# Kernel optimization log

Measured on AMD Instinct MI355X. Metric: run time of the kernel, lower is better.

The kernel has to match this reference:

```python
import jax, jax.numpy as jnp
import numpy as np
import math

HIDDEN = 2048
N_HEADS = 16
N_KV_HEADS = 4
HEAD_DIM = HIDDEN // N_HEADS  # 128
MAX_POS = 4096
ROPE_THETA = 10000.0
B, S = 2, 2048


def _rope_tables():
    freqs = 1.0 / (ROPE_THETA ** (np.arange(0, HEAD_DIM, 2, dtype=np.float32) / HEAD_DIM))
    t = np.arange(MAX_POS, dtype=np.float32)
    f = np.outer(t, freqs)                      # [MAX_POS, HEAD_DIM/2]
    emb = np.concatenate([f, f], axis=-1)       # [MAX_POS, HEAD_DIM]
    return jnp.asarray(np.cos(emb)), jnp.asarray(np.sin(emb))


def setup_inputs() -> dict:
    key = jax.random.key(0)
    ks = jax.random.split(key, 8)
    kv_dim = N_KV_HEADS * HEAD_DIM
    cos, sin = _rope_tables()
    return {
        "hidden_states": jax.random.normal(ks[0], (B, S, HIDDEN), jnp.float32),
        "attention_mask": jnp.zeros((B, S), jnp.float32),
        "position_ids": jnp.arange(S, dtype=jnp.int64 if jax.config.read('jax_enable_x64') else jnp.int32)[None, :],
        "q_w": jax.random.normal(ks[1], (HIDDEN, HIDDEN), jnp.float32) * 0.02,
        "q_b": jnp.zeros((HIDDEN,), jnp.float32),
        "k_w": jax.random.normal(ks[2], (kv_dim, HIDDEN), jnp.float32) * 0.02,
        "k_b": jnp.zeros((kv_dim,), jnp.float32),
        "v_w": jax.random.normal(ks[3], (kv_dim, HIDDEN), jnp.float32) * 0.02,
        "v_b": jnp.zeros((kv_dim,), jnp.float32),
        "o_w": jax.random.normal(ks[4], (HIDDEN, HIDDEN), jnp.float32) * 0.02,
        "cos": cos,
        "sin": sin,
    }


def _rotate_half(x):
    x1, x2 = jnp.split(x, 2, axis=-1)
    return jnp.concatenate([-x2, x1], axis=-1)


def reference(hidden_states, attention_mask, position_ids, q_w, q_b, k_w, k_b,
              v_w, v_b, o_w, cos, sin):
    b, s, _ = hidden_states.shape
    # projections (torch Linear: y = x @ W.T + b)
    q = jnp.einsum('bsi,oi->bso', hidden_states, q_w) + q_b
    k = jnp.einsum('bsi,oi->bso', hidden_states, k_w) + k_b
    v = jnp.einsum('bsi,oi->bso', hidden_states, v_w) + v_b
    q = q.reshape(b, s, N_HEADS, HEAD_DIM).transpose(0, 2, 1, 3)      # [b,h,s,d]
    k = k.reshape(b, s, N_KV_HEADS, HEAD_DIM).transpose(0, 2, 1, 3)   # [b,kv,s,d]
    v = v.reshape(b, s, N_KV_HEADS, HEAD_DIM).transpose(0, 2, 1, 3)
    # RoPE: gather per-position cos/sin, broadcast over heads
    c = cos[position_ids][:, None, :, :]   # [1,1,s,d]
    sn = sin[position_ids][:, None, :, :]
    q = q * c + _rotate_half(q) * sn
    k = k * c + _rotate_half(k) * sn
    # GQA: repeat-interleave kv heads to match query heads
    g = N_HEADS // N_KV_HEADS
    k = jnp.repeat(k, g, axis=1)
    v = jnp.repeat(v, g, axis=1)
    scores = jnp.einsum('bhqd,bhkd->bhqk', q, k) / math.sqrt(HEAD_DIM)
    scores = scores + attention_mask[:, None, None, :]
    attn = jax.nn.softmax(scores.astype(jnp.float32), axis=-1).astype(q.dtype)
    out = jnp.einsum('bhqk,bhkd->bhqd', attn, v)
    out = out.transpose(0, 2, 1, 3).reshape(b, s, HIDDEN)
    return jnp.einsum('bsi,oi->bso', out, o_w)
```

## Files before the change

### kernel.cpp

```cpp
#include <hip/hip_runtime.h>

#define HIDDEN 2048
#define NH 16
#define NKV 4
#define HD 128
#define Bb 2
#define Ss 2048
#define TOK 4096
#define KVD 512
#define LOG2E 1.4426950408889634f
#define QSCALE (0.08838834764831845f * 1.4426950408889634f)
#define DEFER 11.54f

typedef short short8 __attribute__((ext_vector_type(8)));
typedef float f32x4 __attribute__((ext_vector_type(4)));
typedef float f32x16 __attribute__((ext_vector_type(16)));
typedef unsigned int uint4v __attribute__((ext_vector_type(4)));

#define AS1 __attribute__((address_space(1)))
#define AS3 __attribute__((address_space(3)))

#define BARRIER() asm volatile("s_barrier" ::: "memory")
#define WAITV8()  asm volatile("s_waitcnt vmcnt(8)" ::: "memory")
#define WAITV0()  asm volatile("s_waitcnt vmcnt(0)" ::: "memory")

__device__ __forceinline__ float exp2fast(float x){ return __builtin_amdgcn_exp2f(x); }

__device__ __forceinline__ float bf2f(unsigned short u){
  union { unsigned int i; float f; } x; x.i = ((unsigned int)u) << 16; return x.f;
}
__device__ __forceinline__ unsigned short f2bf(float f){
  union { float f; unsigned int i; } x; x.f = f;
  unsigned int r = x.i + 0x7FFFu + ((x.i >> 16) & 1u);
  return (unsigned short)(r >> 16);
}
__device__ __forceinline__ unsigned int cvtpk(float a, float b){
  unsigned int r;
  asm("v_cvt_pk_bf16_f32 %0, %1, %2" : "=v"(r) : "v"(a), "v"(b));
  return r;
}
__device__ __forceinline__ void gld_lds16(const void* g, void* l){
  __builtin_amdgcn_global_load_lds((const AS1 void*)g, (AS3 void*)l, 16, 0, 0);
}

#define R0 2097152
#define R1 3145728
#define R2 3407872
#define R3 3670016
#define R4 4718592
__global__ void cvt_all(const float* __restrict__ s0, const float* __restrict__ s1,
                        const float* __restrict__ s2, const float* __restrict__ s3,
                        const float* __restrict__ s4, unsigned short* __restrict__ dst){
  int i = blockIdx.x * 256 + threadIdx.x;
  const float* src; int off;
  if      (i < R0){ src = s0; off = 0;  }
  else if (i < R1){ src = s1; off = R0; }
  else if (i < R2){ src = s2; off = R1; }
  else if (i < R3){ src = s3; off = R2; }
  else            { src = s4; off = R3; }
  float4 v = reinterpret_cast<const float4*>(src)[i - off];
  ushort4 o;
  o.x = f2bf(v.x); o.y = f2bf(v.y); o.z = f2bf(v.z); o.w = f2bf(v.w);
  reinterpret_cast<ushort4*>(dst)[i] = o;
}

__global__ __launch_bounds__(256, 2) void gemm_nt(
    const unsigned short* __restrict__ A,
    const unsigned short* __restrict__ Bw,
    const float* __restrict__ bias,
    const float* __restrict__ bias2,
    unsigned short* __restrict__ Cb,
    float* __restrict__ Cf,
    unsigned short* __restrict__ vT,
    int M, int N, int K, int ldc)
{
  __shared__ unsigned short lds[2][2][128*64];
  const int tid  = threadIdx.x;
  const int lane = tid & 63;
  const int w  = tid >> 6;
  const int wr = w >> 1, wc = w & 1;
  const int row0 = blockIdx.x * 128;
  const int col0 = blockIdx.y * 128;
  const int fr  = lane & 15;
  const int g16 = lane >> 4;
  const int l8  = lane >> 3;
  const int slot = lane & 7;

  const f32x4 vzero = {0.f, 0.f, 0.f, 0.f};
  f32x4 acc[4][4];
#pragma unroll
  for (int m = 0; m < 4; m++)
#pragma unroll
    for (int n = 0; n < 4; n++) acc[m][n] = vzero;

  auto STAGE = [&](int buf, int kt){
#pragma unroll
    for (int i = 0; i < 4; i++){
      int r = w*32 + i*8 + l8;
      gld_lds16(A  + (size_t)(row0 + r)*K + kt*64 + ((slot ^ (r & 7)) << 3),
                &lds[buf][0][w*2048 + i*512 + lane*8]);
    }
#pragma unroll
    for (int i = 0; i < 4; i++){
      int r = w*32 + i*8 + l8;
      gld_lds16(Bw + (size_t)(col0 + r)*K + kt*64 + ((slot ^ (r & 7)) << 3),
                &lds[buf][1][w*2048 + i*512 + lane*8]);
    }
  };

  const int NT = K >> 6;
  STAGE(0, 0);
  STAGE(1, 1);
  WAITV8();
  BARRIER();

  for (int kt = 0; kt < NT; kt++){
    const int cur = kt & 1;
    const unsigned short* Al = &lds[cur][0][0];
    const unsigned short* Bl = &lds[cur][1][0];
#pragma unroll
    for (int ks = 0; ks < 2; ks++){
      short8 af[4], bf[4];
#pragma unroll
      for (int m = 0; m < 4; m++){
        int r = wr*64 + m*16 + fr;
        af[m] = *(const short8*)&Al[r*64 + (((ks*4 + g16) ^ (r & 7)) << 3)];
      }
#pragma unroll
      for (int n = 0; n < 4; n++){
        int r = wc*64 + n*16 + fr;
        bf[n] = *(const short8*)&Bl[r*64 + (((ks*4 + g16) ^ (r & 7)) << 3)];
      }
      __builtin_amdgcn_s_setprio(1);
#pragma unroll
      for (int m = 0; m < 4; m++)
#pragma unroll
        for (int n = 0; n < 4; n++)
          acc[m][n] = __builtin_amdgcn_mfma_f32_16x16x32_bf16(af[m], bf[n], acc[m][n], 0, 0, 0);
      __builtin_amdgcn_s_setprio(0);
    }
    if (kt == NT - 1) break;
    BARRIER();
    if (kt + 2 < NT){
      STAGE(cur, kt + 2);
      WAITV8();
    } else {
      WAITV0();
    }
    BARRIER();
  }

  const int rr = g16 * 4;
#pragma unroll
  for (int n = 0; n < 4; n++){
    int col = col0 + wc*64 + n*16 + fr;
    float bv = 0.f;
    if (bias) bv = (bias2 && col >= 512) ? bias2[col - 512] : bias[col];
    if (vT && col >= 512){
#pragma unroll
      for (int m = 0; m < 4; m++){
        int row = row0 + wr*64 + m*16 + rr;
        ushort4 pk;
        pk.x = f2bf(acc[m][n][0] + bv); pk.y = f2bf(acc[m][n][1] + bv);
        pk.z = f2bf(acc[m][n][2] + bv); pk.w = f2bf(acc[m][n][3] + bv);
        *reinterpret_cast<ushort4*>(&vT[(size_t)(col - 512) * TOK + row]) = pk;
      }
    } else {
#pragma unroll
      for (int m = 0; m < 4; m++){
        int row = row0 + wr*64 + m*16 + rr;
#pragma unroll
        for (int r = 0; r < 4; r++){
          float v = acc[m][n][r] + bv;
          if (Cf) Cf[(size_t)(row + r) * ldc + col] = v;
          else    Cb[(size_t)(row + r) * ldc + col] = f2bf(v);
        }
      }
    }
  }
}

__global__ void rope_kernel(unsigned short* __restrict__ q, unsigned short* __restrict__ k,
                            const int* __restrict__ pos,
                            const float* __restrict__ cosT, const float* __restrict__ sinT)
{
  int idx = blockIdx.x * blockDim.x + threadIdx.x;
  const int qN = TOK * NH * 64;
  if (idx < qN){
    int d  = idx & 63;
    int hh = (idx >> 6) & (NH - 1);
    int t  = idx >> 10;
    int p  = pos[t & (Ss - 1)];
    float c = cosT[p * HD + d], s = sinT[p * HD + d];
    unsigned short* base = q + (size_t)t * HIDDEN + hh * HD;
    float lo = bf2f(base[d]), hi = bf2f(base[d + 64]);
    base[d]      = f2bf((lo * c - hi * s) * QSCALE);
    base[d + 64] = f2bf((hi * c + lo * s) * QSCALE);
  } else {
    int j  = idx - qN;
    int d  = j & 63;
    int hh = (j >> 6) & (NKV - 1);
    int t  = j >> 8;
    int p  = pos[t & (Ss - 1)];
    float c = cosT[p * HD + d], s = sinT[p * HD + d];
    unsigned short* base = k + (size_t)t * KVD + hh * HD;
    float lo = bf2f(base[d]), hi = bf2f(base[d + 64]);
    base[d]      = f2bf(lo * c - hi * s);
    base[d + 64] = f2bf(hi * c + lo * s);
  }
}

__global__ __launch_bounds__(256, 2) void attn_kernel(
    const unsigned short* __restrict__ Q,
    const unsigned short* __restrict__ Kb,
    const unsigned short* __restrict__ Vt,
    const float* __restrict__ mask,
    unsigned short* __restrict__ O)
{
  __shared__ unsigned short Klds[64*128];
  __shared__ unsigned short Vlds[128*64];

  const int tid = threadIdx.x, lane = tid & 63, wid = tid >> 6;
  const int qt = blockIdx.x, kvh = blockIdx.y, b = blockIdx.z;
  const int head = kvh*4 + wid;
  const int q0 = lane & 31;
  const int h  = lane >> 5;
  const int tokQ = b*Ss + qt*32;

  short8 qf[8];
#pragma unroll
  for (int ds = 0; ds < 8; ds++)
    qf[ds] = *(const short8*)(Q + (size_t)(tokQ + q0)*HIDDEN + head*HD + ds*16 + h*8);

  f32x16 oacc[4];
#pragma unroll
  for (int dblk = 0; dblk < 4; dblk++)
#pragma unroll
    for (int r = 0; r < 16; r++) oacc[dblk][r] = 0.f;
  float mrow = -1e30f, lrow = 0.f;

  const float* maskrow = mask + b*Ss;

  const int kk0 = tid >> 4;
  const int kd  = tid & 15;
  const int dv0 = tid >> 3;
  const int vk  = tid & 7;

  const size_t kgbase = (size_t)(b*Ss)*KVD + (size_t)kvh*HD;
  const size_t vgbase = (size_t)(kvh*HD)*TOK + (size_t)(b*Ss);

  short8 kpre[4], vpre[4];
  auto LOADREG = [&](int tok){
#pragma unroll
    for (int i = 0; i < 4; i++){
      kpre[i] = *(const short8*)(Kb + kgbase + (size_t)(tok + kk0 + i*16)*KVD + kd*8);
      vpre[i] = *(const short8*)(Vt + vgbase + (size_t)(dv0 + i*32)*TOK + tok + vk*8);
    }
  };
  auto WRITELDS = [&](){
#pragma unroll
    for (int i = 0; i < 4; i++){
      int kk = kk0 + i*16;
      *(short8*)&Klds[kk*128 + ((kd*8) ^ ((kk & 7) << 3))] = kpre[i];
      int dv = dv0 + i*32;
      *(short8*)&Vlds[dv*64 + ((vk*8) ^ ((dv & 7) << 3))] = vpre[i];
    }
  };

  const int NT = Ss/64;
  LOADREG(0);

  for (int kt = 0; kt < NT; kt++){
    if (kt) __syncthreads();
    WRITELDS();
    __syncthreads();
    if (kt + 1 < NT) LOADREG((kt + 1)*64);

    f32x16 st0, st1;
#pragma unroll
    for (int r = 0; r < 16; r++){ st0[r] = 0.f; st1[r] = 0.f; }
    __builtin_amdgcn_s_setprio(1);
#pragma unroll
    for (int ds = 0; ds < 8; ds++){
      short8 kf0 = *(const short8*)&Klds[(q0     )*128 + ((ds*16 + h*8) ^ ((q0 & 7) << 3))];
      short8 kf1 = *(const short8*)&Klds[(32 + q0)*128 + ((ds*16 + h*8) ^ ((q0 & 7) << 3))];
      st0 = __builtin_amdgcn_mfma_f32_32x32x16_bf16(kf0, qf[ds], st0, 0, 0, 0);
      st1 = __builtin_amdgcn_mfma_f32_32x32x16_bf16(kf1, qf[ds], st1, 0, 0, 0);
    }
    __builtin_amdgcn_s_setprio(0);

    float p[32];
#pragma unroll
    for (int g2 = 0; g2 < 4; g2++){
      f32x4 m0 = *(const f32x4*)(maskrow + kt*64      + g2*8 + h*4);
      f32x4 m1 = *(const f32x4*)(maskrow + kt*64 + 32 + g2*8 + h*4);
#pragma unroll
      for (int r = 0; r < 4; r++){
        p[g2*4 + r]      = st0[g2*4 + r] + m0[r] * LOG2E;
        p[16 + g2*4 + r] = st1[g2*4 + r] + m1[r] * LOG2E;
      }
    }

    float vmax = p[0];
#pragma unroll
    for (int i = 1; i < 32; i++) vmax = fmaxf(vmax, p[i]);
    vmax = fmaxf(vmax, __shfl_xor(vmax, 32));
    if (__any(vmax > mrow + DEFER)){
      float mnew = fmaxf(mrow, vmax);
      float sc = exp2fast(mrow - mnew);
      mrow = mnew; lrow *= sc;
#pragma unroll
      for (int reg = 0; reg < 16; reg++){
        float scr = __shfl(sc, (reg & 3) + 8*(reg >> 2) + 4*h);
#pragma unroll
        for (int dblk = 0; dblk < 4; dblk++) oacc[dblk][reg] *= scr;
      }
    }
    float rs = 0.f;
#pragma unroll
    for (int i = 0; i < 32; i++){ p[i] = exp2fast(p[i] - mrow); rs += p[i]; }
    rs += __shfl_xor(rs, 32);
    lrow += rs;

    unsigned int pk[8][2];
#pragma unroll
    for (int G = 0; G < 8; G++){
      pk[G][0] = cvtpk(p[G*4 + 0], p[G*4 + 1]);
      pk[G][1] = cvtpk(p[G*4 + 2], p[G*4 + 3]);
    }
    short8 pa[4];
#pragma unroll
    for (int ks = 0; ks < 4; ks++){
      const int ia = 4*(ks >> 1) + 2*(ks & 1);
      unsigned int A0 = pk[ia][0],   A1 = pk[ia][1];
      unsigned int B0 = pk[ia+1][0], B1 = pk[ia+1][1];
      unsigned int s0 = h ? A0 : B0, s1 = h ? A1 : B1;
      unsigned int r0 = (unsigned int)__shfl_xor((int)s0, 32);
      unsigned int r1 = (unsigned int)__shfl_xor((int)s1, 32);
      uint4v w = { h ? r0 : A0, h ? r1 : A1, h ? B0 : r0, h ? B1 : r1 };
      pa[ks] = __builtin_bit_cast(short8, w);
    }

    __builtin_amdgcn_s_setprio(1);
#pragma unroll
    for (int dblk = 0; dblk < 4; dblk++){
#pragma unroll
      for (int ks = 0; ks < 4; ks++){
        short8 vb = *(const short8*)&Vlds[(dblk*32 + q0)*64 + ((ks*16 + h*8) ^ ((q0 & 7) << 3))];
        oacc[dblk] = __builtin_amdgcn_mfma_f32_32x32x16_bf16(pa[ks], vb, oacc[dblk], 0, 0, 0);
      }
    }
    __builtin_amdgcn_s_setprio(0);
  }

  float inv = 1.0f / lrow;
#pragma unroll
  for (int reg = 0; reg < 16; reg++){
    const int crow = (reg & 3) + 8*(reg >> 2) + 4*h;
    float invr = __shfl(inv, crow);
    int row = tokQ + crow;
#pragma unroll
    for (int dblk = 0; dblk < 4; dblk++)
      O[(size_t)row*HIDDEN + head*HD + dblk*32 + q0] = f2bf(oacc[dblk][reg] * invr);
  }
}

extern "C" void kernel_launch(void* const* d_in, const int* in_sizes, int n_in,
                              void* d_out, int out_size, void* d_ws, size_t ws_size,
                              hipStream_t stream)
{
  (void)in_sizes; (void)n_in; (void)out_size; (void)ws_size;
  const float* hs   = (const float*)d_in[0];
  const float* mask = (const float*)d_in[1];
  const int*   pos  = (const int*)d_in[2];
  const float* qw   = (const float*)d_in[3];
  const float* qb   = (const float*)d_in[4];
  const float* kw   = (const float*)d_in[5];
  const float* kb   = (const float*)d_in[6];
  const float* vw   = (const float*)d_in[7];
  const float* vb   = (const float*)d_in[8];
  const float* ow   = (const float*)d_in[9];
  const float* cosT = (const float*)d_in[10];
  const float* sinT = (const float*)d_in[11];
  float* out = (float*)d_out;

  unsigned short* ws  = (unsigned short*)d_ws;
  unsigned short* hsB = ws;
  unsigned short* qwB = hsB + (size_t)TOK * HIDDEN;
  unsigned short* kwB = qwB + (size_t)HIDDEN * HIDDEN;
  unsigned short* vwB = kwB + (size_t)KVD * HIDDEN;
  unsigned short* owB = vwB + (size_t)KVD * HIDDEN;
  unsigned short* qB  = owB + (size_t)HIDDEN * HIDDEN;
  unsigned short* kB  = qB  + (size_t)TOK * HIDDEN;
  unsigned short* vTB = kB  + (size_t)TOK * KVD;
  unsigned short* aoB = vTB + (size_t)KVD * TOK;
  (void)vwB;

  cvt_all<<<R4 / 256, 256, 0, stream>>>(hs, qw, kw, vw, ow, ws);

  gemm_nt<<<dim3(TOK/128, HIDDEN/128), 256, 0, stream>>>(hsB, qwB, qb, nullptr, qB, nullptr, nullptr, TOK, HIDDEN, HIDDEN, HIDDEN);
  gemm_nt<<<dim3(TOK/128, 1024/128),   256, 0, stream>>>(hsB, kwB, kb, vb, kB, nullptr, vTB, TOK, 1024, HIDDEN, KVD);

  {
    int total = TOK * NH * 64 + TOK * NKV * 64;
    rope_kernel<<<total / 256, 256, 0, stream>>>(qB, kB, pos, cosT, sinT);
  }

  attn_kernel<<<dim3(Ss/32, NKV, Bb), 256, 0, stream>>>(qB, kB, vTB, mask, aoB);

  gemm_nt<<<dim3(TOK/128, HIDDEN/128), 256, 0, stream>>>(aoB, owB, nullptr, nullptr, nullptr, out, nullptr, TOK, HIDDEN, HIDDEN, HIDDEN);
}
```

Baseline: 224.3 us.

## Fuse Q and KV projections into one GEMM launch with XCD-aware block swizzle

```diff
diff --git a/kernel.cpp b/kernel.cpp
--- a/kernel.cpp
+++ b/kernel.cpp
@@ -67,11 +67,13 @@
 __global__ __launch_bounds__(256, 2) void gemm_nt(
     const unsigned short* __restrict__ A,
     const unsigned short* __restrict__ Bw,
-    const float* __restrict__ bias,
-    const float* __restrict__ bias2,
-    unsigned short* __restrict__ Cb,
+    const float* __restrict__ qb,
+    const float* __restrict__ kb,
+    const float* __restrict__ vb,
+    unsigned short* __restrict__ CbQ,
+    unsigned short* __restrict__ CbK,
+    unsigned short* __restrict__ vT,
     float* __restrict__ Cf,
-    unsigned short* __restrict__ vT,
     int M, int N, int K, int ldc)
 {
   __shared__ unsigned short lds[2][2][128*64];
@@ -79,8 +81,13 @@
   const int lane = tid & 63;
   const int w  = tid >> 6;
   const int wr = w >> 1, wc = w & 1;
-  const int row0 = blockIdx.x * 128;
-  const int col0 = blockIdx.y * 128;
+
+  const int nwg  = gridDim.x * gridDim.y;
+  const int orig = blockIdx.y * gridDim.x + blockIdx.x;
+  const int swz  = (orig & 7) * (nwg >> 3) + (orig >> 3);
+  const int row0 = (swz & 31) * 128;
+  const int col0 = (swz >> 5) * 128;
+
   const int fr  = lane & 15;
   const int g16 = lane >> 4;
   const int l8  = lane >> 3;
@@ -155,26 +162,41 @@
   for (int n = 0; n < 4; n++){
     int col = col0 + wc*64 + n*16 + fr;
     float bv = 0.f;
-    if (bias) bv = (bias2 && col >= 512) ? bias2[col - 512] : bias[col];
-    if (vT && col >= 512){
+    if (qb) bv = (col < 2048) ? qb[col] : (col < 2560 ? kb[col - 2048] : vb[col - 2560]);
+    if (Cf){
+#pragma unroll
+      for (int m = 0; m < 4; m++){
+        int row = row0 + wr*64 + m*16 + rr;
+#pragma unroll
+        for (int r = 0; r < 4; r++)
+          Cf[(size_t)(row + r) * ldc + col] = acc[m][n][r] + bv;
+      }
+    } else if (col < 2048){
+#pragma unroll
+      for (int m = 0; m < 4; m++){
+        int row = row0 + wr*64 + m*16 + rr;
+#pragma unroll
+        for (int r = 0; r < 4; r++)
+          CbQ[(size_t)(row + r) * 2048 + col] = f2bf(acc[m][n][r] + bv);
+      }
+    } else if (col < 2560){
+      int ck = col - 2048;
+#pragma unroll
+      for (int m = 0; m < 4; m++){
+        int row = row0 + wr*64 + m*16 + rr;
+#pragma unroll
+        for (int r = 0; r < 4; r++)
+          CbK[(size_t)(row + r) * 512 + ck] = f2bf(acc[m][n][r] + bv);
+      }
+    } else {
+      int cv = col - 2560;
 #pragma unroll
       for (int m = 0; m < 4; m++){
         int row = row0 + wr*64 + m*16 + rr;
         ushort4 pk;
         pk.x = f2bf(acc[m][n][0] + bv); pk.y = f2bf(acc[m][n][1] + bv);
         pk.z = f2bf(acc[m][n][2] + bv); pk.w = f2bf(acc[m][n][3] + bv);
-        *reinterpret_cast<ushort4*>(&vT[(size_t)(col - 512) * TOK + row]) = pk;
-      }
-    } else {
-#pragma unroll
-      for (int m = 0; m < 4; m++){
-        int row = row0 + wr*64 + m*16 + rr;
-#pragma unroll
-        for (int r = 0; r < 4; r++){
-          float v = acc[m][n][r] + bv;
-          if (Cf) Cf[(size_t)(row + r) * ldc + col] = v;
-          else    Cb[(size_t)(row + r) * ldc + col] = f2bf(v);
-        }
+        *reinterpret_cast<ushort4*>(&vT[(size_t)cv * TOK + row]) = pk;
       }
     }
   }
@@ -337,8 +359,8 @@
       unsigned int s0 = h ? A0 : B0, s1 = h ? A1 : B1;
       unsigned int r0 = (unsigned int)__shfl_xor((int)s0, 32);
       unsigned int r1 = (unsigned int)__shfl_xor((int)s1, 32);
-      uint4v w = { h ? r0 : A0, h ? r1 : A1, h ? B0 : r0, h ? B1 : r1 };
-      pa[ks] = __builtin_bit_cast(short8, w);
+      uint4v wv = { h ? r0 : A0, h ? r1 : A1, h ? B0 : r0, h ? B1 : r1 };
+      pa[ks] = __builtin_bit_cast(short8, wv);
     }
 
     __builtin_amdgcn_s_setprio(1);
@@ -398,8 +420,8 @@
 
   cvt_all<<<R4 / 256, 256, 0, stream>>>(hs, qw, kw, vw, ow, ws);
 
-  gemm_nt<<<dim3(TOK/128, HIDDEN/128), 256, 0, stream>>>(hsB, qwB, qb, nullptr, qB, nullptr, nullptr, TOK, HIDDEN, HIDDEN, HIDDEN);
-  gemm_nt<<<dim3(TOK/128, 1024/128),   256, 0, stream>>>(hsB, kwB, kb, vb, kB, nullptr, vTB, TOK, 1024, HIDDEN, KVD);
+  gemm_nt<<<dim3(TOK/128, 3072/128), 256, 0, stream>>>(
+      hsB, qwB, qb, kb, vb, qB, kB, vTB, nullptr, TOK, 3072, HIDDEN, 0);
 
   {
     int total = TOK * NH * 64 + TOK * NKV * 64;
@@ -408,5 +430,6 @@
 
   attn_kernel<<<dim3(Ss/32, NKV, Bb), 256, 0, stream>>>(qB, kB, vTB, mask, aoB);
 
-  gemm_nt<<<dim3(TOK/128, HIDDEN/128), 256, 0, stream>>>(aoB, owB, nullptr, nullptr, nullptr, out, nullptr, TOK, HIDDEN, HIDDEN, HIDDEN);
-}
+  gemm_nt<<<dim3(TOK/128, HIDDEN/128), 256, 0, stream>>>(
+      aoB, owB, nullptr, nullptr, nullptr, nullptr, nullptr, nullptr, out, TOK, HIDDEN, HIDDEN, HIDDEN);
+}
```

Measured after the change: 229.5 us. +2.3%, slower.
